# Optimization experiments

Measured on AMD Instinct MI355X. Metric: run time of the kernel, lower is better.

Reference implementation:

```python
import jax, jax.numpy as jnp
import numpy as np

DIM = 3072      # model dim (Qwen-Image)
HEADS = 24
HD = 128        # head dim; inner = HEADS*HD = 3072
INNER = HEADS * HD
FF = 4 * DIM    # 12288
S_IMG = 1024
S_TXT = 256
S_TOT = S_IMG + S_TXT
B = 1
EPS = 1e-6
SCALE_SHIFT = 1.0


def setup_inputs() -> dict:
    key = jax.random.key(0)
    ks = iter(jax.random.split(key, 64))
    W = 0.02

    def nrm(shape, s=W):
        return jax.random.normal(next(ks), shape, dtype=jnp.float32) * s

    # RoPE tables for the joint (txt first, then img) sequence, interleaved layout
    pos = jnp.arange(S_TOT, dtype=jnp.float32)
    inv = 1.0 / (10000.0 ** (jnp.arange(HD // 2, dtype=jnp.float32) / (HD // 2)))
    ang = pos[:, None] * inv[None, :]                       # [S, HD/2]
    rope_cos = jnp.repeat(jnp.cos(ang), 2, axis=-1)         # [S, HD]
    rope_sin = jnp.repeat(jnp.sin(ang), 2, axis=-1)

    inp = {
        "hidden_states": jax.random.normal(next(ks), (B, S_IMG, DIM), dtype=jnp.float32),
        "encoder_hidden_states": jax.random.normal(next(ks), (B, S_TXT, DIM), dtype=jnp.float32),
        "temb": jax.random.normal(next(ks), (B, DIM), dtype=jnp.float32),
        "rope_cos": rope_cos,
        "rope_sin": rope_sin,
        # modulation (AWQW4A16Linear equivalent)
        "img_mod_w": nrm((6 * DIM, DIM)), "img_mod_b": nrm((6 * DIM,)),
        "txt_mod_w": nrm((6 * DIM, DIM)), "txt_mod_b": nrm((6 * DIM,)),
        # attention (SVDQW4A4Linear equivalents)
        "qkv_w": nrm((3 * INNER, DIM)), "qkv_b": nrm((3 * INNER,)),
        "add_qkv_w": nrm((3 * INNER, DIM)), "add_qkv_b": nrm((3 * INNER,)),
        "norm_q_g": jnp.ones((HD,), jnp.float32), "norm_k_g": jnp.ones((HD,), jnp.float32),
        "norm_added_q_g": jnp.ones((HD,), jnp.float32), "norm_added_k_g": jnp.ones((HD,), jnp.float32),
        "to_out_w": nrm((DIM, INNER)), "to_out_b": nrm((DIM,)),
        "to_add_out_w": nrm((DIM, INNER)), "to_add_out_b": nrm((DIM,)),
        # MLPs
        "img_mlp_w1": nrm((FF, DIM)), "img_mlp_b1": nrm((FF,)),
        "img_mlp_w2": nrm((DIM, FF)), "img_mlp_b2": nrm((DIM,)),
        "txt_mlp_w1": nrm((FF, DIM)), "txt_mlp_b1": nrm((FF,)),
        "txt_mlp_w2": nrm((DIM, FF)), "txt_mlp_b2": nrm((DIM,)),
    }
    return inp


def _lin(x, w, b):
    return jnp.matmul(x, w.T) + b


def _ln(x):  # LayerNorm, no affine, eps=1e-6
    mu = jnp.mean(x, axis=-1, keepdims=True)
    var = jnp.mean(jnp.square(x - mu), axis=-1, keepdims=True)
    return (x - mu) * jax.lax.rsqrt(var + EPS)


def _rms(x, g):  # per-head RMSNorm over last dim (HD)
    ms = jnp.mean(jnp.square(x), axis=-1, keepdims=True)
    return x * jax.lax.rsqrt(ms + EPS) * g


def _rope(x, cos, sin):  # x: [B,S,H,D], cos/sin: [S,D], interleaved rotate
    x1 = x[..., 0::2]
    x2 = x[..., 1::2]
    xr = jnp.stack([-x2, x1], axis=-1).reshape(x.shape)
    return x * cos[None, :, None, :] + xr * sin[None, :, None, :]


def _reorder_mod(m):
    # view(B,-1,6).transpose(1,2).reshape(B,-1): de-interleave 6 modulation vecs
    b = m.shape[0]
    return m.reshape(b, DIM, 6).transpose(0, 2, 1).reshape(b, 6 * DIM)


def _modulate(x, mod):
    shift, scale, gate = jnp.split(mod, 3, axis=-1)
    return x * (scale + SCALE_SHIFT)[:, None, :] + shift[:, None, :], gate[:, None, :]


def _mlp(x, w1, b1, w2, b2):  # GELU(tanh) MLP
    h = jax.nn.gelu(_lin(x, w1, b1), approximate=True)
    return _lin(h, w2, b2)


def reference(hidden_states, encoder_hidden_states, temb, rope_cos, rope_sin,
              img_mod_w, img_mod_b, txt_mod_w, txt_mod_b,
              qkv_w, qkv_b, add_qkv_w, add_qkv_b,
              norm_q_g, norm_k_g, norm_added_q_g, norm_added_k_g,
              to_out_w, to_out_b, to_add_out_w, to_add_out_b,
              img_mlp_w1, img_mlp_b1, img_mlp_w2, img_mlp_b2,
              txt_mlp_w1, txt_mlp_b1, txt_mlp_w2, txt_mlp_b2):
    b = hidden_states.shape[0]

    img_mod = _reorder_mod(_lin(jax.nn.silu(temb), img_mod_w, img_mod_b))
    txt_mod = _reorder_mod(_lin(jax.nn.silu(temb), txt_mod_w, txt_mod_b))
    img_mod1, img_mod2 = jnp.split(img_mod, 2, axis=-1)
    txt_mod1, txt_mod2 = jnp.split(txt_mod, 2, axis=-1)

    img_modulated, img_gate1 = _modulate(_ln(hidden_states), img_mod1)
    txt_modulated, txt_gate1 = _modulate(_ln(encoder_hidden_states), txt_mod1)

    # ---- joint attention ----
    img_q, img_k, img_v = jnp.split(_lin(img_modulated, qkv_w, qkv_b), 3, axis=-1)
    txt_q, txt_k, txt_v = jnp.split(_lin(txt_modulated, add_qkv_w, add_qkv_b), 3, axis=-1)

    def heads(x):  # [B,S,INNER] -> [B,S,H,HD]
        return x.reshape(b, x.shape[1], HEADS, HD)

    img_q = _rms(heads(img_q), norm_q_g)
    img_k = _rms(heads(img_k), norm_k_g)
    txt_q = _rms(heads(txt_q), norm_added_q_g)
    txt_k = _rms(heads(txt_k), norm_added_k_g)

    q = jnp.concatenate([txt_q, img_q], axis=1)  # txt first
    k = jnp.concatenate([txt_k, img_k], axis=1)
    v = jnp.concatenate([heads(txt_v), heads(img_v)], axis=1)

    q = _rope(q, rope_cos, rope_sin)
    k = _rope(k, rope_cos, rope_sin)

    scale = 1.0 / jnp.sqrt(jnp.float32(HD))
    scores = jnp.einsum('bqhd,bkhd->bhqk', q, k) * scale
    probs = jax.nn.softmax(scores, axis=-1)
    attn = jnp.einsum('bhqk,bkhd->bqhd', probs, v).reshape(b, S_TOT, INNER)

    txt_attn = attn[:, :S_TXT, :]
    img_attn = attn[:, S_TXT:, :]
    img_attn = _lin(img_attn, to_out_w, to_out_b)
    txt_attn = _lin(txt_attn, to_add_out_w, to_add_out_b)

    hidden_states = hidden_states + img_gate1 * img_attn
    encoder_hidden_states = encoder_hidden_states + txt_gate1 * txt_attn

    # ---- MLPs ----
    img_m2, img_gate2 = _modulate(_ln(hidden_states), img_mod2)
    hidden_states = hidden_states + img_gate2 * _mlp(img_m2, img_mlp_w1, img_mlp_b1, img_mlp_w2, img_mlp_b2)

    txt_m2, txt_gate2 = _modulate(_ln(encoder_hidden_states), txt_mod2)
    encoder_hidden_states = encoder_hidden_states + txt_gate2 * _mlp(txt_m2, txt_mlp_w1, txt_mlp_b1, txt_mlp_w2, txt_mlp_b2)

    return (encoder_hidden_states, hidden_states)
```

## Files before the change

### kernel.cpp

```cpp
#include <hip/hip_runtime.h>

#define DIMC   3072
#define HEADS  24
#define HD     128
#define FF     12288
#define S_IMG  1024
#define S_TXT  256
#define S_TOT  1280
#define EPSF   1e-6f

typedef __attribute__((ext_vector_type(8))) short bf16x8;
typedef __attribute__((ext_vector_type(4))) float f32x4;
typedef __attribute__((ext_vector_type(4))) float float4v;
typedef __attribute__((ext_vector_type(4))) unsigned int u32x4;
typedef __attribute__((ext_vector_type(2))) unsigned int u32x2;

__device__ __forceinline__ unsigned short f2bf(float f) {
    union { float f; unsigned u; } c; c.f = f;
    unsigned u = c.u;
    unsigned r = (u + 0x7fffu + ((u >> 16) & 1u)) >> 16;
    return (unsigned short)r;
}
__device__ __forceinline__ float b2f(unsigned short h) {
    union { unsigned u; float f; } c; c.u = ((unsigned)h) << 16;
    return c.f;
}
__device__ __forceinline__ unsigned packbf(float a, float b) {
    union { float f; unsigned u; } x, y; x.f = a; y.f = b;
    return __builtin_amdgcn_perm(y.u + 0x8000u, x.u + 0x8000u, 0x07060302);
}
__device__ __forceinline__ float gelu_tanh(float v) {
    float u = 1.5957691216057308f * (v + 0.044715f * v * v * v);
    float e = __expf(u);
    float t = 1.0f - 2.0f / (e + 1.0f);
    return 0.5f * v * (1.0f + t);
}

#define GLL16(gsrc, ldst)                                                     \
    __builtin_amdgcn_global_load_lds(                                         \
        (const __attribute__((address_space(1))) void*)(gsrc),                \
        (__attribute__((address_space(3))) void*)(ldst), 16, 0, 0)

struct SwpArgs {
    const float* W;
    const unsigned short* X;
    const float* bias;
    unsigned short* out;
};

template<int EPI>
__global__ __launch_bounds__(512, 2)
void gemm_swp(SwpArgs g0, SwpArgs g1, int nxW, int padx, int K, int ldout)
{
    int bx, sTile;
    SwpArgs g;
    {
        const int id = blockIdx.x;
        const int imgN = padx * 4;
        if (id < imgN) {
            int xcd = id & 7, t = id >> 3;
            int j = t & 3, slot = t >> 2;
            bx = slot * 8 + xcd;
            if (bx >= nxW) return;
            g = g0; sTile = j * 256;
        } else {
            bx = id - imgN;
            g = g1; sTile = 0;
        }
    }
    const int bm = bx * 256;

    __shared__ __align__(16) char smem[131072];
    char* smemW = smem;
    char* smemX = smem + 65536;

    const int tid  = threadIdx.x;
    const int lane = tid & 63;
    const int wave = tid >> 6;
    const int wm = wave >> 2, wc = wave & 3;

    const int pW  = tid & 7;
    const int rW0 = tid >> 3;
    const int swW = (rW0 & 7) << 4;
    const int rX = lane >> 3;
    const int cX = (lane & 7) ^ rX;

    float4v wreg[4][2];

    auto WLOAD = [&](int t) {
        const float* src = g.W + (long)t * 64 + pW * 8;
        #pragma unroll
        for (int i = 0; i < 4; i++) {
            const float* p = src + (long)(bm + rW0 + i * 64) * K;
            wreg[i][0] = *(const float4v*)p;
            wreg[i][1] = *(const float4v*)(p + 4);
        }
    };
    auto WSTORE = [&](int buf) {
        #pragma unroll
        for (int i = 0; i < 4; i++) {
            int r = rW0 + i * 64;
            u32x4 w;
            w[0] = packbf(wreg[i][0][0], wreg[i][0][1]);
            w[1] = packbf(wreg[i][0][2], wreg[i][0][3]);
            w[2] = packbf(wreg[i][1][0], wreg[i][1][1]);
            w[3] = packbf(wreg[i][1][2], wreg[i][1][3]);
            *(u32x4*)(smemW + buf * 32768 + r * 128 + ((pW * 16) ^ swW)) = w;
        }
    };
    auto XSTAGE = [&](int buf, int t) {
        const long kof = (long)t * 64 + cX * 8;
        #pragma unroll
        for (int i = 0; i < 4; i++) {
            int r = i * 64 + wave * 8 + rX;
            GLL16(g.X + (long)(sTile + r) * K + kof,
                  smemX + buf * 32768 + i * 8192 + wave * 1024);
        }
    };

    f32x4 acc[8][4] = {};

    auto RD_W = [&](int buf, int ks, int mh, bf16x8* wf) {
        const int kb = ks * 64 + (lane >> 4) * 16;
        #pragma unroll
        for (int j = 0; j < 4; j++) {
            int r = wm * 128 + (mh * 4 + j) * 16 + (lane & 15);
            wf[j] = *(const bf16x8*)(smemW + buf * 32768 + r * 128 + (kb ^ ((r & 7) << 4)));
        }
    };
    auto RD_X = [&](int buf, int ks, bf16x8* xf) {
        const int kb = ks * 64 + (lane >> 4) * 16;
        #pragma unroll
        for (int j = 0; j < 4; j++) {
            int r = wc * 64 + j * 16 + (lane & 15);
            xf[j] = *(const bf16x8*)(smemX + buf * 32768 + r * 128 + (kb ^ ((r & 7) << 4)));
        }
    };
    auto MFMA16 = [&](int mh, const bf16x8* wf, const bf16x8* xf) {
        #pragma unroll
        for (int j = 0; j < 4; j++)
            #pragma unroll
            for (int ni = 0; ni < 4; ni++)
                acc[mh * 4 + j][ni] = __builtin_amdgcn_mfma_f32_16x16x32_bf16(
                    wf[j], xf[ni], acc[mh * 4 + j][ni], 0, 0, 0);
    };

#define PHASE_SYNC_PRE                                                        \
    __builtin_amdgcn_sched_barrier(0);                                        \
    __builtin_amdgcn_s_barrier();                                             \
    asm volatile("s_waitcnt lgkmcnt(0)" ::: "memory");                        \
    __builtin_amdgcn_sched_barrier(0);                                        \
    __builtin_amdgcn_s_setprio(1);
#define PHASE_SYNC_POST                                                       \
    __builtin_amdgcn_s_setprio(0);                                            \
    __builtin_amdgcn_sched_barrier(0);                                        \
    __builtin_amdgcn_s_barrier();

    const int nk = K >> 6;
    WLOAD(0);
    XSTAGE(0, 0);
    WSTORE(0);
    asm volatile("s_waitcnt vmcnt(0) lgkmcnt(0)" ::: "memory");
    __builtin_amdgcn_sched_barrier(0);
    __builtin_amdgcn_s_barrier();

    for (int t = 0; t < nk; ++t) {
        const int cur = t & 1;
        const bool pf = (t + 1 < nk);
        bf16x8 wf[4], xf[4];

        RD_X(cur, 0, xf);
        RD_W(cur, 0, 0, wf);
        if (pf) WLOAD(t + 1);
        PHASE_SYNC_PRE
        MFMA16(0, wf, xf);
        PHASE_SYNC_POST

        RD_W(cur, 0, 1, wf);
        if (pf) XSTAGE(cur ^ 1, t + 1);
        PHASE_SYNC_PRE
        MFMA16(1, wf, xf);
        PHASE_SYNC_POST

        RD_X(cur, 1, xf);
        RD_W(cur, 1, 0, wf);
        PHASE_SYNC_PRE
        MFMA16(0, wf, xf);
        PHASE_SYNC_POST

        RD_W(cur, 1, 1, wf);
        if (pf) WSTORE(cur ^ 1);
        PHASE_SYNC_PRE
        MFMA16(1, wf, xf);
        __builtin_amdgcn_s_setprio(0);
        __builtin_amdgcn_sched_barrier(0);
        asm volatile("s_waitcnt vmcnt(0)" ::: "memory");
        __builtin_amdgcn_sched_barrier(0);
        __builtin_amdgcn_s_barrier();
    }
#undef PHASE_SYNC_PRE
#undef PHASE_SYNC_POST

    #pragma unroll
    for (int mi = 0; mi < 8; mi++) {
        int m0 = wm * 128 + mi * 16 + ((lane >> 4) << 2);
        float4v bv = *(const float4v*)(g.bias + bm + m0);
        #pragma unroll
        for (int ni = 0; ni < 4; ni++) {
            int n = wc * 64 + ni * 16 + (lane & 15);
            float v0 = acc[mi][ni][0] + bv[0];
            float v1 = acc[mi][ni][1] + bv[1];
            float v2 = acc[mi][ni][2] + bv[2];
            float v3 = acc[mi][ni][3] + bv[3];
            if constexpr (EPI == 2) {
                v0 = gelu_tanh(v0); v1 = gelu_tanh(v1);
                v2 = gelu_tanh(v2); v3 = gelu_tanh(v3);
            }
            u32x2 w;
            w[0] = packbf(v0, v1);
            w[1] = packbf(v2, v3);
            *(u32x2*)(smem + n * 512 + ((2 * m0) ^ ((n & 31) << 4))) = w;
        }
    }
    __syncthreads();
    {
        const int s = tid >> 1;
        const int cbase = (tid & 1) * 16;
        unsigned short* orow = g.out + (long)(sTile + s) * ldout + bm;
        #pragma unroll
        for (int c = 0; c < 16; c++) {
            int chunk = cbase + c;
            u32x4 d = *(const u32x4*)(smem + s * 512 + ((chunk * 16) ^ ((s & 31) << 4)));
            *(u32x4*)(orow + chunk * 8) = d;
        }
    }
}

struct GemmArgs {
    const unsigned short* A;
    const void* B;
    const float* bias;
    void* out;
    long bOut;
};

template<int EPI, bool BF16B, bool SWZ>
__global__ __launch_bounds__(256)
void gemm_bt(GemmArgs g0, GemmArgs g1, int ysplit,
             int K, int lda, int ldb, int ldout,
             long batchA, long batchB, int nbn, int nby)
{
    int by, bnIdx, z;
    if constexpr (SWZ) {
        const int id = blockIdx.x;
        const int xcd = id & 7, t = id >> 3;
        const int j = t % 10;
        const int slot = t / 10;
        const int gidx = slot * 8 + xcd;
        by = j; bnIdx = gidx % nbn; z = gidx / nbn;
        (void)nby;
    } else {
        by = blockIdx.y; bnIdx = blockIdx.x; z = blockIdx.z;
    }

    __shared__ __align__(16) char smem[65536];
    char* smemA = smem;
    char* smemB = smem + 32768;

    const int tid  = threadIdx.x;
    const int lane = tid & 63;
    const int wave = tid >> 6;
    const int wm = wave >> 1, wc = wave & 1;

    const bool second = (by >= ysplit);
    const GemmArgs g = second ? g1 : g0;
    const int bm = (second ? by - ysplit : by) * 128;
    const int bn = bnIdx * 128;

    const unsigned short* A = g.A + (long)z * batchA;
    const float* Bf = (const float*)g.B + (long)z * batchB;
    const unsigned short* Bh = (const unsigned short*)g.B + (long)z * batchB;

    const int rA = lane >> 3;
    const int cA = (lane & 7) ^ rA;
    const int pB = tid & 7;
    const int rB0 = tid >> 3;
    const int swB = (rB0 & 7) << 4;

    float4v breg[4][2];

    auto BLOAD = [&](int t) {
        const float* src = Bf + (long)t * 64 + pB * 8;
        #pragma unroll
        for (int i = 0; i < 4; i++) {
            const float* p = src + (long)(bn + rB0 + i * 32) * ldb;
            breg[i][0] = *(const float4v*)p;
            breg[i][1] = *(const float4v*)(p + 4);
        }
    };
    auto STAGE_A = [&](int buf, int t) {
        const long kof = (long)t * 64 + cA * 8;
        #pragma unroll
        for (int i = 0; i < 4; i++) {
            int r = i * 32 + wave * 8 + rA;
            GLL16(A + (long)(bm + r) * lda + kof,
                  smemA + buf * 16384 + i * 4096 + wave * 1024);
        }
    };
    auto STAGE_B16 = [&](int buf, int t) {
        const long kof = (long)t * 64 + cA * 8;
        #pragma unroll
        for (int i = 0; i < 4; i++) {
            int r = i * 32 + wave * 8 + rA;
            GLL16(Bh + (long)(bn + r) * ldb + kof,
                  smemB + buf * 16384 + i * 4096 + wave * 1024);
        }
    };
    auto BSTORE = [&](int buf) {
        #pragma unroll
        for (int i = 0; i < 4; i++) {
            int r = rB0 + i * 32;
            u32x4 w;
            w[0] = packbf(breg[i][0][0], breg[i][0][1]);
            w[1] = packbf(breg[i][0][2], breg[i][0][3]);
            w[2] = packbf(breg[i][1][0], breg[i][1][1]);
            w[3] = packbf(breg[i][1][2], breg[i][1][3]);
            *(u32x4*)(smemB + buf * 16384 + r * 128 + ((pB * 16) ^ swB)) = w;
        }
    };

    f32x4 acc[4][4] = {};
    auto COMPUTE = [&](int buf) {
        #pragma unroll
        for (int ks = 0; ks < 2; ks++) {
            const int kb = ks * 64 + (lane >> 4) * 16;
            bf16x8 af[4], bfr[4];
            #pragma unroll
            for (int mi = 0; mi < 4; mi++) {
                int r = wm * 64 + mi * 16 + (lane & 15);
                af[mi] = *(const bf16x8*)(smemA + buf * 16384 + r * 128 + (kb ^ ((r & 7) << 4)));
            }
            #pragma unroll
            for (int ni = 0; ni < 4; ni++) {
                int r = wc * 64 + ni * 16 + (lane & 15);
                bfr[ni] = *(const bf16x8*)(smemB + buf * 16384 + r * 128 + (kb ^ ((r & 7) << 4)));
            }
            #pragma unroll
            for (int mi = 0; mi < 4; mi++)
                #pragma unroll
                for (int ni = 0; ni < 4; ni++)
                    acc[mi][ni] = __builtin_amdgcn_mfma_f32_16x16x32_bf16(
                        af[mi], bfr[ni], acc[mi][ni], 0, 0, 0);
        }
    };

    const int nk = K >> 6;
    if constexpr (BF16B) {
        STAGE_A(0, 0); STAGE_B16(0, 0);
    } else {
        BLOAD(0); STAGE_A(0, 0); BSTORE(0);
    }
    __syncthreads();
    for (int t = 0; t < nk; ++t) {
        const int cur = t & 1;
        if (t + 1 < nk) {
            if constexpr (BF16B) {
                STAGE_A(cur ^ 1, t + 1); STAGE_B16(cur ^ 1, t + 1);
            } else {
                BLOAD(t + 1); STAGE_A(cur ^ 1, t + 1);
            }
        }
        __builtin_amdgcn_sched_barrier(0);
        COMPUTE(cur);
        __builtin_amdgcn_sched_barrier(0);
        if constexpr (!BF16B) { if (t + 1 < nk) BSTORE(cur ^ 1); }
        __syncthreads();
    }

    unsigned short* outh = (unsigned short*)g.out + (long)z * g.bOut;
    float*          outf = (float*)g.out + (long)z * g.bOut;
    #pragma unroll
    for (int mi = 0; mi < 4; mi++) {
        #pragma unroll
        for (int ni = 0; ni < 4; ni++) {
            int n = bn + wc * 64 + ni * 16 + (lane & 15);
            float bv = g.bias ? g.bias[n] : 0.0f;
            #pragma unroll
            for (int r = 0; r < 4; r++) {
                int m = bm + wm * 64 + mi * 16 + (lane >> 4) * 4 + r;
                float v = acc[mi][ni][r] + bv;
                long o = (long)m * ldout + n;
                if constexpr (EPI == 0)      outf[o] = v;
                else                         outh[o] = f2bf(v);
            }
        }
    }
}

__global__ void silu_k(const float* __restrict__ x, float* __restrict__ out) {
    int i = blockIdx.x * 256 + threadIdx.x;
    if (i < DIMC) { float v = x[i]; out[i] = v / (1.0f + expf(-v)); }
}

__global__ __launch_bounds__(256)
void mod_gemv(const float* __restrict__ st,
              const float* __restrict__ Wimg, const float* __restrict__ bimg,
              const float* __restrict__ Wtxt, const float* __restrict__ btxt,
              float* __restrict__ mimg, float* __restrict__ mtxt)
{
    int wv = threadIdx.x >> 6, lane = threadIdx.x & 63;
    int r = blockIdx.x * 4 + wv;
    const float* W = blockIdx.y ? Wtxt : Wimg;
    const float* b = blockIdx.y ? btxt : bimg;
    float* out = blockIdx.y ? mtxt : mimg;
    const float* row = W + (long)r * DIMC;
    float acc = 0.f;
    #pragma unroll
    for (int j = 0; j < 12; j++) {
        float4v wvv = ((const float4v*)row)[lane + j * 64];
        float4v xv  = ((const float4v*)st)[lane + j * 64];
        acc += wvv[0] * xv[0] + wvv[1] * xv[1] + wvv[2] * xv[2] + wvv[3] * xv[3];
    }
    #pragma unroll
    for (int o = 32; o; o >>= 1) acc += __shfl_xor(acc, o);
    if (lane == 0) {
        int d = r / 6, j6 = r % 6;
        out[j6 * DIMC + d] = acc + b[r];
    }
}

__global__ __launch_bounds__(256)
void ln_mod(const float* __restrict__ x, const float* __restrict__ shift,
            const float* __restrict__ scale, unsigned short* __restrict__ out)
{
    __shared__ float red[8];
    long row = blockIdx.x;
    const float* xr = x + row * DIMC;
    float4v v[3];
    float sum = 0.f, sq = 0.f;
    #pragma unroll
    for (int j = 0; j < 3; j++) {
        v[j] = ((const float4v*)xr)[threadIdx.x + j * 256];
        #pragma unroll
        for (int c = 0; c < 4; c++) { sum += v[j][c]; sq += v[j][c] * v[j][c]; }
    }
    int lane = threadIdx.x & 63, wv = threadIdx.x >> 6;
    #pragma unroll
    for (int o = 32; o; o >>= 1) { sum += __shfl_xor(sum, o); sq += __shfl_xor(sq, o); }
    if (lane == 0) { red[wv] = sum; red[4 + wv] = sq; }
    __syncthreads();
    sum = red[0] + red[1] + red[2] + red[3];
    sq  = red[4] + red[5] + red[6] + red[7];
    float mu = sum / DIMC;
    float var = sq / DIMC - mu * mu;
    float rstd = rsqrtf(var + EPSF);
    #pragma unroll
    for (int j = 0; j < 3; j++) {
        int nb = (threadIdx.x + j * 256) * 4;
        #pragma unroll
        for (int c = 0; c < 4; c++) {
            int n = nb + c;
            float y = (v[j][c] - mu) * rstd * (scale[n] + 1.0f) + shift[n];
            out[row * DIMC + n] = f2bf(y);
        }
    }
}

__global__ __launch_bounds__(256)
void reduce_ln(const float* __restrict__ p0, const float* __restrict__ p1,
               const float* __restrict__ pbias, const float* __restrict__ base,
               const float* __restrict__ gate1, const float* __restrict__ shift2,
               const float* __restrict__ scale2,
               float* __restrict__ h1, unsigned short* __restrict__ mA)
{
    __shared__ float red[8];
    long off = (long)blockIdx.x * DIMC;
    float4v v[3];
    float sum = 0.f, sq = 0.f;
    #pragma unroll
    for (int j = 0; j < 3; j++) {
        int idx = threadIdx.x + j * 256;
        float4v a  = ((const float4v*)(base + off))[idx];
        float4v q0 = ((const float4v*)(p0 + off))[idx];
        float4v q1 = ((const float4v*)(p1 + off))[idx];
        float4v gb = ((const float4v*)pbias)[idx];
        float4v gt = ((const float4v*)gate1)[idx];
        #pragma unroll
        for (int c = 0; c < 4; c++) {
            float val = a[c] + gt[c] * (gb[c] + q0[c] + q1[c]);
            v[j][c] = val; sum += val; sq += val * val;
        }
        ((float4v*)(h1 + off))[idx] = v[j];
    }
    int lane = threadIdx.x & 63, wv = threadIdx.x >> 6;
    #pragma unroll
    for (int o = 32; o; o >>= 1) { sum += __shfl_xor(sum, o); sq += __shfl_xor(sq, o); }
    if (lane == 0) { red[wv] = sum; red[4 + wv] = sq; }
    __syncthreads();
    sum = red[0] + red[1] + red[2] + red[3];
    sq  = red[4] + red[5] + red[6] + red[7];
    float mu = sum / DIMC;
    float rstd = rsqrtf(sq / DIMC - mu * mu + EPSF);
    #pragma unroll
    for (int j = 0; j < 3; j++) {
        int nb = (threadIdx.x + j * 256) * 4;
        #pragma unroll
        for (int c = 0; c < 4; c++) {
            int n = nb + c;
            float y = (v[j][c] - mu) * rstd * (scale2[n] + 1.0f) + shift2[n];
            mA[off + n] = f2bf(y);
        }
    }
}

__global__ __launch_bounds__(256)
void reduce_out(const float* __restrict__ p, long PS,
                const float* __restrict__ h1, const float* __restrict__ wbias,
                const float* __restrict__ gate2, float* __restrict__ out, int n4)
{
    int i = blockIdx.x * 256 + threadIdx.x;
    if (i >= n4) return;
    int n = (i * 4) % DIMC;
    float4v s = ((const float4v*)p)[i];
    float4v s1 = ((const float4v*)(p + PS))[i];
    float4v s2 = ((const float4v*)(p + 2 * PS))[i];
    float4v s3 = ((const float4v*)(p + 3 * PS))[i];
    float4v h = ((const float4v*)h1)[i];
    float4v bv = *(const float4v*)(wbias + n);
    float4v gv = *(const float4v*)(gate2 + n);
    float4v r;
    #pragma unroll
    for (int c = 0; c < 4; c++)
        r[c] = h[c] + gv[c] * (bv[c] + s[c] + s1[c] + s2[c] + s3[c]);
    ((float4v*)out)[i] = r;
}

__global__ __launch_bounds__(256)
void qkv_post(const unsigned short* __restrict__ qkv_img,
              const unsigned short* __restrict__ qkv_txt,
              const float* __restrict__ nqg, const float* __restrict__ nkg,
              const float* __restrict__ naqg, const float* __restrict__ nakg,
              const float* __restrict__ rc, const float* __restrict__ rs,
              unsigned short* __restrict__ q, unsigned short* __restrict__ k,
              unsigned short* __restrict__ vt)
{
    int s = blockIdx.x;
    int h = blockIdx.y * 4 + (threadIdx.x >> 6);
    int d0 = threadIdx.x & 63;
    const unsigned short* src;
    const float *gq, *gk;
    if (s < S_TXT) { src = qkv_txt + (long)s * 3 * DIMC; gq = naqg; gk = nakg; }
    else           { src = qkv_img + (long)(s - S_TXT) * 3 * DIMC; gq = nqg; gk = nkg; }

    float q0 = b2f(src[h * HD + d0]),            q1 = b2f(src[h * HD + d0 + 64]);
    float k0 = b2f(src[DIMC + h * HD + d0]),     k1 = b2f(src[DIMC + h * HD + d0 + 64]);
    float v0 = b2f(src[2 * DIMC + h * HD + d0]), v1 = b2f(src[2 * DIMC + h * HD + d0 + 64]);

    float sqq = q0 * q0 + q1 * q1;
    float sqk = k0 * k0 + k1 * k1;
    #pragma unroll
    for (int o = 32; o; o >>= 1) { sqq += __shfl_xor(sqq, o); sqk += __shfl_xor(sqk, o); }
    float rq = rsqrtf(sqq / (float)HD + EPSF);
    float rk = rsqrtf(sqk / (float)HD + EPSF);
    q0 *= rq * gq[d0]; q1 *= rq * gq[d0 + 64];
    k0 *= rk * gk[d0]; k1 *= rk * gk[d0 + 64];

    float qp0 = __shfl_xor(q0, 1), qp1 = __shfl_xor(q1, 1);
    float kp0 = __shfl_xor(k0, 1), kp1 = __shfl_xor(k1, 1);
    float c0 = rc[(long)s * HD + d0], c1 = rc[(long)s * HD + d0 + 64];
    float s0 = rs[(long)s * HD + d0], s1 = rs[(long)s * HD + d0 + 64];
    float sgn = (d0 & 1) ? 1.0f : -1.0f;
    float qo0 = q0 * c0 + sgn * qp0 * s0;
    float qo1 = q1 * c1 + sgn * qp1 * s1;
    float ko0 = k0 * c0 + sgn * kp0 * s0;
    float ko1 = k1 * c1 + sgn * kp1 * s1;

    const float scl = 0.08838834764831845f;
    long qkbase = ((long)h * S_TOT + s) * HD;
    q[qkbase + d0]      = f2bf(qo0 * scl);
    q[qkbase + d0 + 64] = f2bf(qo1 * scl);
    k[qkbase + d0]      = f2bf(ko0);
    k[qkbase + d0 + 64] = f2bf(ko1);
    vt[((long)h * HD + d0) * S_TOT + s]        = f2bf(v0);
    vt[((long)h * HD + d0 + 64) * S_TOT + s]   = f2bf(v1);
}

__global__ __launch_bounds__(256)
void softmax_k(unsigned short* __restrict__ scores)
{
    long row = (long)blockIdx.x * 4 + (threadIdx.x >> 6);
    int lane = threadIdx.x & 63;
    unsigned short* p = scores + row * S_TOT;
    float v[20];
    float mx = -1e30f;
    #pragma unroll
    for (int j = 0; j < 20; j++) { v[j] = b2f(p[lane + j * 64]); mx = fmaxf(mx, v[j]); }
    #pragma unroll
    for (int o = 32; o; o >>= 1) mx = fmaxf(mx, __shfl_xor(mx, o));
    float sum = 0.f;
    #pragma unroll
    for (int j = 0; j < 20; j++) { v[j] = __expf(v[j] - mx); sum += v[j]; }
    #pragma unroll
    for (int o = 32; o; o >>= 1) sum += __shfl_xor(sum, o);
    float inv = 1.0f / sum;
    #pragma unroll
    for (int j = 0; j < 20; j++) p[lane + j * 64] = f2bf(v[j] * inv);
}

extern "C" void kernel_launch(void* const* d_in, const int* in_sizes, int n_in,
                              void* d_out, int out_size, void* d_ws, size_t ws_size,
                              hipStream_t stream)
{
    const float* hidden   = (const float*)d_in[0];
    const float* enc      = (const float*)d_in[1];
    const float* temb     = (const float*)d_in[2];
    const float* rope_cos = (const float*)d_in[3];
    const float* rope_sin = (const float*)d_in[4];
    const float* img_mod_w = (const float*)d_in[5];
    const float* img_mod_b = (const float*)d_in[6];
    const float* txt_mod_w = (const float*)d_in[7];
    const float* txt_mod_b = (const float*)d_in[8];
    const float* qkv_w     = (const float*)d_in[9];
    const float* qkv_b     = (const float*)d_in[10];
    const float* add_qkv_w = (const float*)d_in[11];
    const float* add_qkv_b = (const float*)d_in[12];
    const float* norm_q_g  = (const float*)d_in[13];
    const float* norm_k_g  = (const float*)d_in[14];
    const float* norm_aq_g = (const float*)d_in[15];
    const float* norm_ak_g = (const float*)d_in[16];
    const float* to_out_w  = (const float*)d_in[17];
    const float* to_out_b  = (const float*)d_in[18];
    const float* to_add_out_w = (const float*)d_in[19];
    const float* to_add_out_b = (const float*)d_in[20];
    const float* img_mlp_w1 = (const float*)d_in[21];
    const float* img_mlp_b1 = (const float*)d_in[22];
    const float* img_mlp_w2 = (const float*)d_in[23];
    const float* img_mlp_b2 = (const float*)d_in[24];
    const float* txt_mlp_w1 = (const float*)d_in[25];
    const float* txt_mlp_b1 = (const float*)d_in[26];
    const float* txt_mlp_w2 = (const float*)d_in[27];
    const float* txt_mlp_b2 = (const float*)d_in[28];

    char* w = (char*)d_ws;
    auto alloc = [&](size_t bytes) { char* p = w; w += (bytes + 255) & ~(size_t)255; return p; };
    float* silu_t  = (float*)alloc(DIMC * 4);
    float* mod_img = (float*)alloc(6 * DIMC * 4);
    float* mod_txt = (float*)alloc(6 * DIMC * 4);
    unsigned short* mA_img = (unsigned short*)alloc((long)S_IMG * DIMC * 2);
    unsigned short* mA_txt = (unsigned short*)alloc((long)S_TXT * DIMC * 2);
    unsigned short* qkv_img = (unsigned short*)alloc((long)S_IMG * 3 * DIMC * 2);
    unsigned short* qkv_txt = (unsigned short*)alloc((long)S_TXT * 3 * DIMC * 2);
    unsigned short* qb = (unsigned short*)alloc((long)HEADS * S_TOT * HD * 2);
    unsigned short* kb = (unsigned short*)alloc((long)HEADS * S_TOT * HD * 2);
    unsigned short* vt = (unsigned short*)alloc((long)HEADS * HD * S_TOT * 2);
    unsigned short* scores = (unsigned short*)alloc((long)HEADS * S_TOT * S_TOT * 2);
    unsigned short* attn = (unsigned short*)alloc((long)S_TOT * DIMC * 2);
    float* h1_img = (float*)alloc((long)S_IMG * DIMC * 4);
    float* h1_txt = (float*)alloc((long)S_TXT * DIMC * 4);
    unsigned short* gelu_img = (unsigned short*)alloc((long)S_IMG * FF * 2);
    unsigned short* gelu_txt = (unsigned short*)alloc((long)S_TXT * FF * 2);

    const long PS = (long)S_TOT * DIMC;
    float* part = (float*)scores;
    float* part_img = part;
    float* part_txt = part + (long)S_IMG * DIMC;

    float* out_enc = (float*)d_out;
    float* out_hid = (float*)d_out + (long)S_TXT * DIMC;

    silu_k<<<12, 256, 0, stream>>>(temb, silu_t);
    mod_gemv<<<dim3(4608, 2), 256, 0, stream>>>(silu_t, img_mod_w, img_mod_b,
                                                txt_mod_w, txt_mod_b, mod_img, mod_txt);

    ln_mod<<<S_IMG, 256, 0, stream>>>(hidden, mod_img, mod_img + DIMC, mA_img);
    ln_mod<<<S_TXT, 256, 0, stream>>>(enc, mod_txt, mod_txt + DIMC, mA_txt);

    {
        SwpArgs gi{qkv_w, mA_img, qkv_b, qkv_img};
        SwpArgs gt{add_qkv_w, mA_txt, add_qkv_b, qkv_txt};
        gemm_swp<1><<<40 * 4 + 36, 512, 0, stream>>>(gi, gt, 36, 40, DIMC, 3 * DIMC);
    }

    qkv_post<<<dim3(S_TOT, HEADS / 4), 256, 0, stream>>>(
        qkv_img, qkv_txt, norm_q_g, norm_k_g, norm_aq_g, norm_ak_g,
        rope_cos, rope_sin, qb, kb, vt);

    {
        GemmArgs gs{qb, kb, nullptr, scores, (long)S_TOT * S_TOT};
        gemm_bt<1, true, false><<<dim3(10, 10, HEADS), 256, 0, stream>>>(
            gs, gs, 10, HD, HD, HD, S_TOT,
            (long)S_TOT * HD, (long)S_TOT * HD, 0, 0);
    }
    softmax_k<<<(HEADS * S_TOT) / 4, 256, 0, stream>>>(scores);
    {
        GemmArgs gp{scores, vt, nullptr, attn, HD};
        gemm_bt<1, true, false><<<dim3(1, 10, HEADS), 256, 0, stream>>>(
            gp, gp, 10, S_TOT, S_TOT, S_TOT, DIMC,
            (long)S_TOT * S_TOT, (long)HD * S_TOT, 0, 0);
    }

    {
        GemmArgs gi{attn + (long)S_TXT * DIMC, to_out_w, nullptr, part_img, PS};
        GemmArgs gt{attn, to_add_out_w, nullptr, part_txt, PS};
        gemm_bt<0, false, true><<<24 * 2 * 10, 256, 0, stream>>>(
            gi, gt, 8, 1536, DIMC, DIMC, DIMC, 1536, 1536, 24, 10);
    }

    reduce_ln<<<S_IMG, 256, 0, stream>>>(
        part_img, part_img + PS, to_out_b, hidden,
        mod_img + 2 * DIMC, mod_img + 3 * DIMC, mod_img + 4 * DIMC,
        h1_img, mA_img);
    reduce_ln<<<S_TXT, 256, 0, stream>>>(
        part_txt, part_txt + PS, to_add_out_b, enc,
        mod_txt + 2 * DIMC, mod_txt + 3 * DIMC, mod_txt + 4 * DIMC,
        h1_txt, mA_txt);

    {
        SwpArgs gi{img_mlp_w1, mA_img, img_mlp_b1, gelu_img};
        SwpArgs gt{txt_mlp_w1, mA_txt, txt_mlp_b1, gelu_txt};
        gemm_swp<2><<<48 * 4 + 48, 512, 0, stream>>>(gi, gt, 48, 48, DIMC, FF);
    }

    {
        GemmArgs gi{gelu_img, img_mlp_w2, nullptr, part_img, PS};
        GemmArgs gt{gelu_txt, txt_mlp_w2, nullptr, part_txt, PS};
        gemm_bt<0, false, true><<<24 * 4 * 10, 256, 0, stream>>>(
            gi, gt, 8, 3072, FF, FF, DIMC, 3072, 3072, 24, 10);
    }
    reduce_out<<<(S_IMG * DIMC / 4 + 255) / 256, 256, 0, stream>>>(
        part_img, PS, h1_img, img_mlp_b2, mod_img + 5 * DIMC, out_hid,
        S_IMG * DIMC / 4);
    reduce_out<<<(S_TXT * DIMC / 4 + 255) / 256, 256, 0, stream>>>(
        part_txt, PS, h1_txt, txt_mlp_b2, mod_txt + 5 * DIMC, out_enc,
        S_TXT * DIMC / 4);
}
```

Baseline: 768.8 us.

## Route output and MLP-down projections through split-K 256-tile swp GEMM with bf16 partials

The to_out and MLP w2 projections move from the 128x128 gemm_bt kernel onto the larger 256x256 software-pipelined gemm_swp kernel, using a 4-way split-K over blockIdx.y (previously 2-way for to_out). Partial sums are now written as bf16 instead of fp32, and the reduce kernels sum four bf16 partials. The intent is better weight reuse and MFMA throughput from larger tiles, plus less partial-sum traffic. In exchange, rounding partials to bf16 loses accuracy, and the extra split-K partial for to_out adds reduction work.

```diff
diff --git a/kernel.cpp b/kernel.cpp
--- a/kernel.cpp
+++ b/kernel.cpp
@@ -50,7 +50,8 @@
 
 template<int EPI>
 __global__ __launch_bounds__(512, 2)
-void gemm_swp(SwpArgs g0, SwpArgs g1, int nxW, int padx, int K, int ldout)
+void gemm_swp(SwpArgs g0, SwpArgs g1, int nxW, int padx,
+              int K, int ld, int ldout, long pOut)
 {
     int bx, sTile;
     SwpArgs g;
@@ -69,6 +70,9 @@
         }
     }
     const int bm = bx * 256;
+    const int z = blockIdx.y;
+    const float* Wp = g.W + (long)z * K;
+    const unsigned short* Xp = g.X + (long)z * K;
 
     __shared__ __align__(16) char smem[131072];
     char* smemW = smem;
@@ -88,10 +92,10 @@
     float4v wreg[4][2];
 
     auto WLOAD = [&](int t) {
-        const float* src = g.W + (long)t * 64 + pW * 8;
+        const float* src = Wp + (long)t * 64 + pW * 8;
         #pragma unroll
         for (int i = 0; i < 4; i++) {
-            const float* p = src + (long)(bm + rW0 + i * 64) * K;
+            const float* p = src + (long)(bm + rW0 + i * 64) * ld;
             wreg[i][0] = *(const float4v*)p;
             wreg[i][1] = *(const float4v*)(p + 4);
         }
@@ -113,7 +117,7 @@
         #pragma unroll
         for (int i = 0; i < 4; i++) {
             int r = i * 64 + wave * 8 + rX;
-            GLL16(g.X + (long)(sTile + r) * K + kof,
+            GLL16(Xp + (long)(sTile + r) * ld + kof,
                   smemX + buf * 32768 + i * 8192 + wave * 1024);
         }
     };
@@ -204,7 +208,8 @@
     #pragma unroll
     for (int mi = 0; mi < 8; mi++) {
         int m0 = wm * 128 + mi * 16 + ((lane >> 4) << 2);
-        float4v bv = *(const float4v*)(g.bias + bm + m0);
+        float4v bv = {0.f, 0.f, 0.f, 0.f};
+        if (g.bias) bv = *(const float4v*)(g.bias + bm + m0);
         #pragma unroll
         for (int ni = 0; ni < 4; ni++) {
             int n = wc * 64 + ni * 16 + (lane & 15);
@@ -226,7 +231,7 @@
     {
         const int s = tid >> 1;
         const int cbase = (tid & 1) * 16;
-        unsigned short* orow = g.out + (long)(sTile + s) * ldout + bm;
+        unsigned short* orow = g.out + (long)z * pOut + (long)(sTile + s) * ldout + bm;
         #pragma unroll
         for (int c = 0; c < 16; c++) {
             int chunk = cbase + c;
@@ -244,24 +249,13 @@
     long bOut;
 };
 
-template<int EPI, bool BF16B, bool SWZ>
+template<int EPI>
 __global__ __launch_bounds__(256)
-void gemm_bt(GemmArgs g0, GemmArgs g1, int ysplit,
-             int K, int lda, int ldb, int ldout,
-             long batchA, long batchB, int nbn, int nby)
-{
-    int by, bnIdx, z;
-    if constexpr (SWZ) {
-        const int id = blockIdx.x;
-        const int xcd = id & 7, t = id >> 3;
-        const int j = t % 10;
-        const int slot = t / 10;
-        const int gidx = slot * 8 + xcd;
-        by = j; bnIdx = gidx % nbn; z = gidx / nbn;
-        (void)nby;
-    } else {
-        by = blockIdx.y; bnIdx = blockIdx.x; z = blockIdx.z;
-    }
+void gemm_att(GemmArgs g0, GemmArgs g1, int ysplit,
+              int K, int lda, int ldb, int ldout,
+              long batchA, long batchB)
+{
+    const int by = blockIdx.y, bnIdx = blockIdx.x, z = blockIdx.z;
 
     __shared__ __align__(16) char smem[65536];
     char* smemA = smem;
@@ -278,26 +272,11 @@
     const int bn = bnIdx * 128;
 
     const unsigned short* A = g.A + (long)z * batchA;
-    const float* Bf = (const float*)g.B + (long)z * batchB;
     const unsigned short* Bh = (const unsigned short*)g.B + (long)z * batchB;
 
     const int rA = lane >> 3;
     const int cA = (lane & 7) ^ rA;
-    const int pB = tid & 7;
-    const int rB0 = tid >> 3;
-    const int swB = (rB0 & 7) << 4;
-
-    float4v breg[4][2];
-
-    auto BLOAD = [&](int t) {
-        const float* src = Bf + (long)t * 64 + pB * 8;
-        #pragma unroll
-        for (int i = 0; i < 4; i++) {
-            const float* p = src + (long)(bn + rB0 + i * 32) * ldb;
-            breg[i][0] = *(const float4v*)p;
-            breg[i][1] = *(const float4v*)(p + 4);
-        }
-    };
+
     auto STAGE_A = [&](int buf, int t) {
         const long kof = (long)t * 64 + cA * 8;
         #pragma unroll
@@ -307,25 +286,13 @@
                   smemA + buf * 16384 + i * 4096 + wave * 1024);
         }
     };
-    auto STAGE_B16 = [&](int buf, int t) {
+    auto STAGE_B = [&](int buf, int t) {
         const long kof = (long)t * 64 + cA * 8;
         #pragma unroll
         for (int i = 0; i < 4; i++) {
             int r = i * 32 + wave * 8 + rA;
             GLL16(Bh + (long)(bn + r) * ldb + kof,
                   smemB + buf * 16384 + i * 4096 + wave * 1024);
-        }
-    };
-    auto BSTORE = [&](int buf) {
-        #pragma unroll
-        for (int i = 0; i < 4; i++) {
-            int r = rB0 + i * 32;
-            u32x4 w;
-            w[0] = packbf(breg[i][0][0], breg[i][0][1]);
-            w[1] = packbf(breg[i][0][2], breg[i][0][3]);
-            w[2] = packbf(breg[i][1][0], breg[i][1][1]);
-            w[3] = packbf(breg[i][1][2], breg[i][1][3]);
-            *(u32x4*)(smemB + buf * 16384 + r * 128 + ((pB * 16) ^ swB)) = w;
         }
     };
 
@@ -355,43 +322,27 @@
     };
 
     const int nk = K >> 6;
-    if constexpr (BF16B) {
-        STAGE_A(0, 0); STAGE_B16(0, 0);
-    } else {
-        BLOAD(0); STAGE_A(0, 0); BSTORE(0);
-    }
+    STAGE_A(0, 0); STAGE_B(0, 0);
     __syncthreads();
     for (int t = 0; t < nk; ++t) {
         const int cur = t & 1;
-        if (t + 1 < nk) {
-            if constexpr (BF16B) {
-                STAGE_A(cur ^ 1, t + 1); STAGE_B16(cur ^ 1, t + 1);
-            } else {
-                BLOAD(t + 1); STAGE_A(cur ^ 1, t + 1);
-            }
-        }
+        if (t + 1 < nk) { STAGE_A(cur ^ 1, t + 1); STAGE_B(cur ^ 1, t + 1); }
         __builtin_amdgcn_sched_barrier(0);
         COMPUTE(cur);
         __builtin_amdgcn_sched_barrier(0);
-        if constexpr (!BF16B) { if (t + 1 < nk) BSTORE(cur ^ 1); }
         __syncthreads();
     }
 
     unsigned short* outh = (unsigned short*)g.out + (long)z * g.bOut;
-    float*          outf = (float*)g.out + (long)z * g.bOut;
     #pragma unroll
     for (int mi = 0; mi < 4; mi++) {
         #pragma unroll
         for (int ni = 0; ni < 4; ni++) {
             int n = bn + wc * 64 + ni * 16 + (lane & 15);
-            float bv = g.bias ? g.bias[n] : 0.0f;
             #pragma unroll
             for (int r = 0; r < 4; r++) {
                 int m = bm + wm * 64 + mi * 16 + (lane >> 4) * 4 + r;
-                float v = acc[mi][ni][r] + bv;
-                long o = (long)m * ldout + n;
-                if constexpr (EPI == 0)      outf[o] = v;
-                else                         outh[o] = f2bf(v);
+                outh[(long)m * ldout + n] = f2bf(acc[mi][ni][r]);
             }
         }
     }
@@ -467,7 +418,7 @@
 }
 
 __global__ __launch_bounds__(256)
-void reduce_ln(const float* __restrict__ p0, const float* __restrict__ p1,
+void reduce_ln(const unsigned short* __restrict__ p, long PSu,
                const float* __restrict__ pbias, const float* __restrict__ base,
                const float* __restrict__ gate1, const float* __restrict__ shift2,
                const float* __restrict__ scale2,
@@ -481,13 +432,19 @@
     for (int j = 0; j < 3; j++) {
         int idx = threadIdx.x + j * 256;
         float4v a  = ((const float4v*)(base + off))[idx];
-        float4v q0 = ((const float4v*)(p0 + off))[idx];
-        float4v q1 = ((const float4v*)(p1 + off))[idx];
         float4v gb = ((const float4v*)pbias)[idx];
         float4v gt = ((const float4v*)gate1)[idx];
+        float ps[4] = {gb[0], gb[1], gb[2], gb[3]};
+        const unsigned short* pr = p + off + idx * 4;
+        #pragma unroll
+        for (int z = 0; z < 4; z++) {
+            const unsigned short* q = pr + z * PSu;
+            ps[0] += b2f(q[0]); ps[1] += b2f(q[1]);
+            ps[2] += b2f(q[2]); ps[3] += b2f(q[3]);
+        }
         #pragma unroll
         for (int c = 0; c < 4; c++) {
-            float val = a[c] + gt[c] * (gb[c] + q0[c] + q1[c]);
+            float val = a[c] + gt[c] * ps[c];
             v[j][c] = val; sum += val; sq += val * val;
         }
         ((float4v*)(h1 + off))[idx] = v[j];
@@ -514,24 +471,28 @@
 }
 
 __global__ __launch_bounds__(256)
-void reduce_out(const float* __restrict__ p, long PS,
+void reduce_out(const unsigned short* __restrict__ p, long PSu,
                 const float* __restrict__ h1, const float* __restrict__ wbias,
                 const float* __restrict__ gate2, float* __restrict__ out, int n4)
 {
     int i = blockIdx.x * 256 + threadIdx.x;
     if (i >= n4) return;
     int n = (i * 4) % DIMC;
-    float4v s = ((const float4v*)p)[i];
-    float4v s1 = ((const float4v*)(p + PS))[i];
-    float4v s2 = ((const float4v*)(p + 2 * PS))[i];
-    float4v s3 = ((const float4v*)(p + 3 * PS))[i];
+    float ps[4] = {0.f, 0.f, 0.f, 0.f};
+    const unsigned short* pr = p + (long)i * 4;
+    #pragma unroll
+    for (int z = 0; z < 4; z++) {
+        const unsigned short* q = pr + z * PSu;
+        ps[0] += b2f(q[0]); ps[1] += b2f(q[1]);
+        ps[2] += b2f(q[2]); ps[3] += b2f(q[3]);
+    }
     float4v h = ((const float4v*)h1)[i];
     float4v bv = *(const float4v*)(wbias + n);
     float4v gv = *(const float4v*)(gate2 + n);
     float4v r;
     #pragma unroll
     for (int c = 0; c < 4; c++)
-        r[c] = h[c] + gv[c] * (bv[c] + s[c] + s1[c] + s2[c] + s3[c]);
+        r[c] = h[c] + gv[c] * (bv[c] + ps[c]);
     ((float4v*)out)[i] = r;
 }
 
@@ -660,10 +621,9 @@
     unsigned short* gelu_img = (unsigned short*)alloc((long)S_IMG * FF * 2);
     unsigned short* gelu_txt = (unsigned short*)alloc((long)S_TXT * FF * 2);
 
-    const long PS = (long)S_TOT * DIMC;
-    float* part = (float*)scores;
-    float* part_img = part;
-    float* part_txt = part + (long)S_IMG * DIMC;
+    const long PSu = (long)S_TOT * DIMC;
+    unsigned short* partu = scores;
+    unsigned short* part_txt = partu + (long)S_IMG * DIMC;
 
     float* out_enc = (float*)d_out;
     float* out_hid = (float*)d_out + (long)S_TXT * DIMC;
@@ -678,7 +638,8 @@
     {
         SwpArgs gi{qkv_w, mA_img, qkv_b, qkv_img};
         SwpArgs gt{add_qkv_w, mA_txt, add_qkv_b, qkv_txt};
-        gemm_swp<1><<<40 * 4 + 36, 512, 0, stream>>>(gi, gt, 36, 40, DIMC, 3 * DIMC);
+        gemm_swp<1><<<dim3(40 * 4 + 36, 1), 512, 0, stream>>>(
+            gi, gt, 36, 40, DIMC, DIMC, 3 * DIMC, 0);
     }
 
     qkv_post<<<dim3(S_TOT, HEADS / 4), 256, 0, stream>>>(
@@ -687,50 +648,51 @@
 
     {
         GemmArgs gs{qb, kb, nullptr, scores, (long)S_TOT * S_TOT};
-        gemm_bt<1, true, false><<<dim3(10, 10, HEADS), 256, 0, stream>>>(
+        gemm_att<1><<<dim3(10, 10, HEADS), 256, 0, stream>>>(
             gs, gs, 10, HD, HD, HD, S_TOT,
-            (long)S_TOT * HD, (long)S_TOT * HD, 0, 0);
+            (long)S_TOT * HD, (long)S_TOT * HD);
     }
     softmax_k<<<(HEADS * S_TOT) / 4, 256, 0, stream>>>(scores);
     {
         GemmArgs gp{scores, vt, nullptr, attn, HD};
-        gemm_bt<1, true, false><<<dim3(1, 10, HEADS), 256, 0, stream>>>(
+        gemm_att<1><<<dim3(1, 10, HEADS), 256, 0, stream>>>(
             gp, gp, 10, S_TOT, S_TOT, S_TOT, DIMC,
-            (long)S_TOT * S_TOT, (long)HD * S_TOT, 0, 0);
-    }
-
-    {
-        GemmArgs gi{attn + (long)S_TXT * DIMC, to_out_w, nullptr, part_img, PS};
-        GemmArgs gt{attn, to_add_out_w, nullptr, part_txt, PS};
-        gemm_bt<0, false, true><<<24 * 2 * 10, 256, 0, stream>>>(
-            gi, gt, 8, 1536, DIMC, DIMC, DIMC, 1536, 1536, 24, 10);
+            (long)S_TOT * S_TOT, (long)HD * S_TOT);
+    }
+
+    {
+        SwpArgs gi{to_out_w, attn + (long)S_TXT * DIMC, nullptr, partu};
+        SwpArgs gt{to_add_out_w, attn, nullptr, part_txt};
+        gemm_swp<0><<<dim3(16 * 4 + 12, 4), 512, 0, stream>>>(
+            gi, gt, 12, 16, 768, DIMC, DIMC, PSu);
     }
 
     reduce_ln<<<S_IMG, 256, 0, stream>>>(
-        part_img, part_img + PS, to_out_b, hidden,
+        partu, PSu, to_out_b, hidden,
         mod_img + 2 * DIMC, mod_img + 3 * DIMC, mod_img + 4 * DIMC,
         h1_img, mA_img);
     reduce_ln<<<S_TXT, 256, 0, stream>>>(
-        part_txt, part_txt + PS, to_add_out_b, enc,
+        part_txt, PSu, to_add_out_b, enc,
         mod_txt + 2 * DIMC, mod_txt + 3 * DIMC, mod_txt + 4 * DIMC,
         h1_txt, mA_txt);
 
     {
         SwpArgs gi{img_mlp_w1, mA_img, img_mlp_b1, gelu_img};
         SwpArgs gt{txt_mlp_w1, mA_txt, txt_mlp_b1, gelu_txt};
-        gemm_swp<2><<<48 * 4 + 48, 512, 0, stream>>>(gi, gt, 48, 48, DIMC, FF);
-    }
-
-    {
-        GemmArgs gi{gelu_img, img_mlp_w2, nullptr, part_img, PS};
-        GemmArgs gt{gelu_txt, txt_mlp_w2, nullptr, part_txt, PS};
-        gemm_bt<0, false, true><<<24 * 4 * 10, 256, 0, stream>>>(
-            gi, gt, 8, 3072, FF, FF, DIMC, 3072, 3072, 24, 10);
+        gemm_swp<2><<<dim3(48 * 4 + 48, 1), 512, 0, stream>>>(
+            gi, gt, 48, 48, DIMC, DIMC, FF, 0);
+    }
+
+    {
+        SwpArgs gi{img_mlp_w2, gelu_img, nullptr, partu};
+        SwpArgs gt{txt_mlp_w2, gelu_txt, nullptr, part_txt};
+        gemm_swp<0><<<dim3(16 * 4 + 12, 4), 512, 0, stream>>>(
+            gi, gt, 12, 16, 3072, FF, DIMC, PSu);
     }
     reduce_out<<<(S_IMG * DIMC / 4 + 255) / 256, 256, 0, stream>>>(
-        part_img, PS, h1_img, img_mlp_b2, mod_img + 5 * DIMC, out_hid,
+        partu, PSu, h1_img, img_mlp_b2, mod_img + 5 * DIMC, out_hid,
         S_IMG * DIMC / 4);
     reduce_out<<<(S_TXT * DIMC / 4 + 255) / 256, 256, 0, stream>>>(
-        part_txt, PS, h1_txt, txt_mlp_b2, mod_txt + 5 * DIMC, out_enc,
+        part_txt, PSu, h1_txt, txt_mlp_b2, mod_txt + 5 * DIMC, out_enc,
         S_TXT * DIMC / 4);
 }
```

After: 871.8 us. +13.4%, slower.

## Use K=32 tiles with half shared memory for fp32-weight split-K GEMMs

Applied to the files above, without the earlier changes.

The split-K GEMMs that read fp32 weights (attention output projection and MLP down projection) now run through a new kernel with K-step 32 instead of 64. This halves shared memory to 32KB and sets launch bounds for 5 blocks per CU, with a new swizzle for the narrower 64-byte rows. The goal is more resident blocks to hide the latency of global fp32 weight loads. The attention bf16 GEMMs move to a separate specialised kernel with the bias and fp32 paths removed. In exchange there are twice as many loop iterations and barriers per tile, and register pressure may rise under the tighter launch bound.

```diff
diff --git a/kernel.cpp b/kernel.cpp
--- a/kernel.cpp
+++ b/kernel.cpp
@@ -244,28 +244,23 @@
     long bOut;
 };
 
-template<int EPI, bool BF16B, bool SWZ>
-__global__ __launch_bounds__(256)
-void gemm_bt(GemmArgs g0, GemmArgs g1, int ysplit,
-             int K, int lda, int ldb, int ldout,
-             long batchA, long batchB, int nbn, int nby)
-{
-    int by, bnIdx, z;
-    if constexpr (SWZ) {
-        const int id = blockIdx.x;
-        const int xcd = id & 7, t = id >> 3;
-        const int j = t % 10;
-        const int slot = t / 10;
-        const int gidx = slot * 8 + xcd;
-        by = j; bnIdx = gidx % nbn; z = gidx / nbn;
-        (void)nby;
-    } else {
-        by = blockIdx.y; bnIdx = blockIdx.x; z = blockIdx.z;
-    }
-
-    __shared__ __align__(16) char smem[65536];
+template<int EPI>
+__global__ __launch_bounds__(256, 5)
+void gemm_bt32(GemmArgs g0, GemmArgs g1, int ysplit,
+               int K, int lda, int ldb, int ldout,
+               long batchA, long batchB, int nbn)
+{
+    const int id = blockIdx.x;
+    const int xcd = id & 7, t = id >> 3;
+    const int by = t % 10;
+    const int slot = t / 10;
+    const int gidx = slot * 8 + xcd;
+    const int bnIdx = gidx % nbn;
+    const int z = gidx / nbn;
+
+    __shared__ __align__(16) char smem[32768];
     char* smemA = smem;
-    char* smemB = smem + 32768;
+    char* smemB = smem + 16384;
 
     const int tid  = threadIdx.x;
     const int lane = tid & 63;
@@ -279,25 +274,133 @@
 
     const unsigned short* A = g.A + (long)z * batchA;
     const float* Bf = (const float*)g.B + (long)z * batchB;
-    const unsigned short* Bh = (const unsigned short*)g.B + (long)z * batchB;
+
+    const int rA_in = lane >> 2;
+    const int sA = (rA_in & 3) ^ ((lane >> 4) & 3);
+    const int cA = (lane & 3) ^ sA;
+
+    const int rB = tid >> 1;
+    const int hB = tid & 1;
+    const int sB = (rB & 3) ^ ((rB >> 2) & 3);
+
+    float4v breg[4];
+
+    auto BLOAD = [&](int t) {
+        const float* p = Bf + (long)(bn + rB) * ldb + (long)t * 32 + hB * 16;
+        breg[0] = *(const float4v*)p;
+        breg[1] = *(const float4v*)(p + 4);
+        breg[2] = *(const float4v*)(p + 8);
+        breg[3] = *(const float4v*)(p + 12);
+    };
+    auto STAGE_A = [&](int buf, int t) {
+        const long kof = (long)t * 32 + cA * 8;
+        #pragma unroll
+        for (int i = 0; i < 2; i++) {
+            int r = i * 64 + wave * 16 + rA_in;
+            GLL16(A + (long)(bm + r) * lda + kof,
+                  smemA + buf * 8192 + i * 4096 + wave * 1024);
+        }
+    };
+    auto BSTORE = [&](int buf) {
+        u32x4 w0, w1;
+        w0[0] = packbf(breg[0][0], breg[0][1]);
+        w0[1] = packbf(breg[0][2], breg[0][3]);
+        w0[2] = packbf(breg[1][0], breg[1][1]);
+        w0[3] = packbf(breg[1][2], breg[1][3]);
+        w1[0] = packbf(breg[2][0], breg[2][1]);
+        w1[1] = packbf(breg[2][2], breg[2][3]);
+        w1[2] = packbf(breg[3][0], breg[3][1]);
+        w1[3] = packbf(breg[3][2], breg[3][3]);
+        char* base = smemB + buf * 8192 + rB * 64;
+        *(u32x4*)(base + (((2 * hB) ^ sB) * 16))     = w0;
+        *(u32x4*)(base + (((2 * hB + 1) ^ sB) * 16)) = w1;
+    };
+
+    f32x4 acc[4][4] = {};
+    const int sRd = (lane & 3) ^ ((lane >> 2) & 3);
+    const int kc  = ((lane >> 4) ^ sRd) & 3;
+
+    auto COMPUTE = [&](int buf) {
+        bf16x8 af[4], bfr[4];
+        #pragma unroll
+        for (int mi = 0; mi < 4; mi++) {
+            int r = wm * 64 + mi * 16 + (lane & 15);
+            af[mi] = *(const bf16x8*)(smemA + buf * 8192 + r * 64 + kc * 16);
+        }
+        #pragma unroll
+        for (int ni = 0; ni < 4; ni++) {
+            int r = wc * 64 + ni * 16 + (lane & 15);
+            bfr[ni] = *(const bf16x8*)(smemB + buf * 8192 + r * 64 + kc * 16);
+        }
+        #pragma unroll
+        for (int mi = 0; mi < 4; mi++)
+            #pragma unroll
+            for (int ni = 0; ni < 4; ni++)
+                acc[mi][ni] = __builtin_amdgcn_mfma_f32_16x16x32_bf16(
+                    af[mi], bfr[ni], acc[mi][ni], 0, 0, 0);
+    };
+
+    const int nk = K >> 5;
+    BLOAD(0); STAGE_A(0, 0); BSTORE(0);
+    __syncthreads();
+    for (int t = 0; t < nk; ++t) {
+        const int cur = t & 1;
+        if (t + 1 < nk) {
+            BLOAD(t + 1); STAGE_A(cur ^ 1, t + 1);
+        }
+        __builtin_amdgcn_sched_barrier(0);
+        COMPUTE(cur);
+        __builtin_amdgcn_sched_barrier(0);
+        if (t + 1 < nk) BSTORE(cur ^ 1);
+        __syncthreads();
+    }
+
+    float* outf = (float*)g.out + (long)z * g.bOut;
+    #pragma unroll
+    for (int mi = 0; mi < 4; mi++) {
+        #pragma unroll
+        for (int ni = 0; ni < 4; ni++) {
+            int n = bn + wc * 64 + ni * 16 + (lane & 15);
+            #pragma unroll
+            for (int r = 0; r < 4; r++) {
+                int m = bm + wm * 64 + mi * 16 + (lane >> 4) * 4 + r;
+                outf[(long)m * ldout + n] = acc[mi][ni][r];
+            }
+        }
+    }
+}
+
+struct AttArgs {
+    const unsigned short* A;
+    const unsigned short* B;
+    unsigned short* out;
+    long bOut;
+};
+
+__global__ __launch_bounds__(256)
+void gemm_att(AttArgs g, int K, int lda, int ldb, int ldout,
+              long batchA, long batchB)
+{
+    const int by = blockIdx.y, bnIdx = blockIdx.x, z = blockIdx.z;
+
+    __shared__ __align__(16) char smem[65536];
+    char* smemA = smem;
+    char* smemB = smem + 32768;
+
+    const int tid  = threadIdx.x;
+    const int lane = tid & 63;
+    const int wave = tid >> 6;
+    const int wm = wave >> 1, wc = wave & 1;
+
+    const int bm = by * 128;
+    const int bn = bnIdx * 128;
+
+    const unsigned short* A = g.A + (long)z * batchA;
+    const unsigned short* Bh = g.B + (long)z * batchB;
 
     const int rA = lane >> 3;
     const int cA = (lane & 7) ^ rA;
-    const int pB = tid & 7;
-    const int rB0 = tid >> 3;
-    const int swB = (rB0 & 7) << 4;
-
-    float4v breg[4][2];
-
-    auto BLOAD = [&](int t) {
-        const float* src = Bf + (long)t * 64 + pB * 8;
-        #pragma unroll
-        for (int i = 0; i < 4; i++) {
-            const float* p = src + (long)(bn + rB0 + i * 32) * ldb;
-            breg[i][0] = *(const float4v*)p;
-            breg[i][1] = *(const float4v*)(p + 4);
-        }
-    };
+
     auto STAGE_A = [&](int buf, int t) {
         const long kof = (long)t * 64 + cA * 8;
         #pragma unroll
@@ -307,25 +410,13 @@
                   smemA + buf * 16384 + i * 4096 + wave * 1024);
         }
     };
-    auto STAGE_B16 = [&](int buf, int t) {
+    auto STAGE_B = [&](int buf, int t) {
         const long kof = (long)t * 64 + cA * 8;
         #pragma unroll
         for (int i = 0; i < 4; i++) {
             int r = i * 32 + wave * 8 + rA;
             GLL16(Bh + (long)(bn + r) * ldb + kof,
                   smemB + buf * 16384 + i * 4096 + wave * 1024);
-        }
-    };
-    auto BSTORE = [&](int buf) {
-        #pragma unroll
-        for (int i = 0; i < 4; i++) {
-            int r = rB0 + i * 32;
-            u32x4 w;
-            w[0] = packbf(breg[i][0][0], breg[i][0][1]);
-            w[1] = packbf(breg[i][0][2], breg[i][0][3]);
-            w[2] = packbf(breg[i][1][0], breg[i][1][1]);
-            w[3] = packbf(breg[i][1][2], breg[i][1][3]);
-            *(u32x4*)(smemB + buf * 16384 + r * 128 + ((pB * 16) ^ swB)) = w;
         }
     };
 
@@ -355,43 +446,27 @@
     };
 
     const int nk = K >> 6;
-    if constexpr (BF16B) {
-        STAGE_A(0, 0); STAGE_B16(0, 0);
-    } else {
-        BLOAD(0); STAGE_A(0, 0); BSTORE(0);
-    }
+    STAGE_A(0, 0); STAGE_B(0, 0);
     __syncthreads();
     for (int t = 0; t < nk; ++t) {
         const int cur = t & 1;
-        if (t + 1 < nk) {
-            if constexpr (BF16B) {
-                STAGE_A(cur ^ 1, t + 1); STAGE_B16(cur ^ 1, t + 1);
-            } else {
-                BLOAD(t + 1); STAGE_A(cur ^ 1, t + 1);
-            }
-        }
+        if (t + 1 < nk) { STAGE_A(cur ^ 1, t + 1); STAGE_B(cur ^ 1, t + 1); }
         __builtin_amdgcn_sched_barrier(0);
         COMPUTE(cur);
         __builtin_amdgcn_sched_barrier(0);
-        if constexpr (!BF16B) { if (t + 1 < nk) BSTORE(cur ^ 1); }
         __syncthreads();
     }
 
-    unsigned short* outh = (unsigned short*)g.out + (long)z * g.bOut;
-    float*          outf = (float*)g.out + (long)z * g.bOut;
+    unsigned short* outh = g.out + (long)z * g.bOut;
     #pragma unroll
     for (int mi = 0; mi < 4; mi++) {
         #pragma unroll
         for (int ni = 0; ni < 4; ni++) {
             int n = bn + wc * 64 + ni * 16 + (lane & 15);
-            float bv = g.bias ? g.bias[n] : 0.0f;
             #pragma unroll
             for (int r = 0; r < 4; r++) {
                 int m = bm + wm * 64 + mi * 16 + (lane >> 4) * 4 + r;
-                float v = acc[mi][ni][r] + bv;
-                long o = (long)m * ldout + n;
-                if constexpr (EPI == 0)      outf[o] = v;
-                else                         outh[o] = f2bf(v);
+                outh[(long)m * ldout + n] = f2bf(acc[mi][ni][r]);
             }
         }
     }
@@ -686,24 +761,23 @@
         rope_cos, rope_sin, qb, kb, vt);
 
     {
-        GemmArgs gs{qb, kb, nullptr, scores, (long)S_TOT * S_TOT};
-        gemm_bt<1, true, false><<<dim3(10, 10, HEADS), 256, 0, stream>>>(
-            gs, gs, 10, HD, HD, HD, S_TOT,
-            (long)S_TOT * HD, (long)S_TOT * HD, 0, 0);
+        AttArgs gs{qb, kb, scores, (long)S_TOT * S_TOT};
+        gemm_att<<<dim3(10, 10, HEADS), 256, 0, stream>>>(
+            gs, HD, HD, HD, S_TOT, (long)S_TOT * HD, (long)S_TOT * HD);
     }
     softmax_k<<<(HEADS * S_TOT) / 4, 256, 0, stream>>>(scores);
     {
-        GemmArgs gp{scores, vt, nullptr, attn, HD};
-        gemm_bt<1, true, false><<<dim3(1, 10, HEADS), 256, 0, stream>>>(
-            gp, gp, 10, S_TOT, S_TOT, S_TOT, DIMC,
-            (long)S_TOT * S_TOT, (long)HD * S_TOT, 0, 0);
+        AttArgs gp{scores, vt, attn, HD};
+        gemm_att<<<dim3(1, 10, HEADS), 256, 0, stream>>>(
+            gp, S_TOT, S_TOT, S_TOT, DIMC,
+            (long)S_TOT * S_TOT, (long)HD * S_TOT);
     }
 
     {
         GemmArgs gi{attn + (long)S_TXT * DIMC, to_out_w, nullptr, part_img, PS};
         GemmArgs gt{attn, to_add_out_w, nullptr, part_txt, PS};
-        gemm_bt<0, false, true><<<24 * 2 * 10, 256, 0, stream>>>(
-            gi, gt, 8, 1536, DIMC, DIMC, DIMC, 1536, 1536, 24, 10);
+        gemm_bt32<0><<<24 * 2 * 10, 256, 0, stream>>>(
+            gi, gt, 8, 1536, DIMC, DIMC, DIMC, 1536, 1536, 24);
     }
 
     reduce_ln<<<S_IMG, 256, 0, stream>>>(
@@ -724,8 +798,8 @@
     {
         GemmArgs gi{gelu_img, img_mlp_w2, nullptr, part_img, PS};
         GemmArgs gt{gelu_txt, txt_mlp_w2, nullptr, part_txt, PS};
-        gemm_bt<0, false, true><<<24 * 4 * 10, 256, 0, stream>>>(
-            gi, gt, 8, 3072, FF, FF, DIMC, 3072, 3072, 24, 10);
+        gemm_bt32<0><<<24 * 4 * 10, 256, 0, stream>>>(
+            gi, gt, 8, 3072, FF, FF, DIMC, 3072, 3072, 24);
     }
     reduce_out<<<(S_IMG * DIMC / 4 + 255) / 256, 256, 0, stream>>>(
         part_img, PS, h1_img, img_mlp_b2, mod_img + 5 * DIMC, out_hid,
```

After: 1.404 ms. +82.6%, slower.
